# Performance work log

Hardware: AMD Instinct MI355X
Metric: run time of the kernel (lower is better)

Reference implementation:

```python
import jax, jax.numpy as jnp
import numpy as np

B, D1, N, F_IN, F_OUT = 8, 16, 2048, 64, 64


def setup_inputs() -> dict:
    key = jax.random.key(0)
    k1, k2, k3 = jax.random.split(key, 3)
    x = jax.random.normal(k1, (B, D1, N, F_IN), dtype=jnp.float32)
    adj = jax.random.uniform(k2, (B, N, N), dtype=jnp.float32)
    weight = jax.random.normal(k3, (F_IN, F_OUT), dtype=jnp.float32) * (1.0 / np.sqrt(F_IN))
    return {"x": x, "adj": adj, "weight": weight}


def reference(x, adj, weight):
    # x: [B, D1, N, F_in], adj: [B, N, N], weight: [F_in, F_out]
    # Original: per (b, i) loops -> support = x[b,i] @ W; out[b,i] = adj[b] @ support
    # Fused as batched einsums. Note: the module's bias parameter is unused in forward.
    support = jnp.einsum('binf,fg->bing', x, weight)          # feature transform
    out = jnp.einsum('bnm,bimg->bing', adj, support)           # adjacency aggregation
    return out
```

## Files before the change

kernel.cpp:

```cpp
#include <hip/hip_runtime.h>
#include <hip/hip_bf16.h>

typedef __attribute__((ext_vector_type(8))) short bf16x8;
typedef __attribute__((ext_vector_type(4))) float f32x4;

#define NB    8
#define ND1   16
#define NN    2048
#define NF    64
#define GN    1024

__device__ static inline ushort f2bf(float f) {
    unsigned int u = __builtin_bit_cast(unsigned int, f);
    unsigned int r = (u + 0x7FFFu + ((u >> 16) & 1u)) >> 16;
    return (ushort)r;
}

__device__ static inline void gload_lds16(const void* g, void* l) {
    __builtin_amdgcn_global_load_lds(
        (const __attribute__((address_space(1))) void*)g,
        (__attribute__((address_space(3))) void*)l, 16, 0, 0);
}

__global__ __launch_bounds__(256) void prep_kernel(
    const float* __restrict__ x, const float* __restrict__ w,
    const float* __restrict__ adj, ushort* __restrict__ sT,
    ushort* __restrict__ adjb)
{
    __shared__ __align__(16) char smem[16384 + 16640];
    int t = threadIdx.x;

    if (blockIdx.x < 2048) {
        int idx = blockIdx.x * 256 + t;
        const int stride = 2048 * 256;
        const float4* a4 = (const float4*)adj;
        uint4* o4 = (uint4*)adjb;
        const int n8 = NB * NN * NN / 8;
        for (int i = idx; i < n8; i += stride) {
            float4 v0 = a4[2 * i];
            float4 v1 = a4[2 * i + 1];
            union { uint4 q; ushort u[8]; } p;
            p.u[0] = f2bf(v0.x); p.u[1] = f2bf(v0.y);
            p.u[2] = f2bf(v0.z); p.u[3] = f2bf(v0.w);
            p.u[4] = f2bf(v1.x); p.u[5] = f2bf(v1.y);
            p.u[6] = f2bf(v1.z); p.u[7] = f2bf(v1.w);
            o4[i] = p.q;
        }
        return;
    }

    float*  Ws = (float*)smem;
    float*  xs = (float*)(smem + 16384);
    ushort* tr = (ushort*)(smem + 16384);

    int bid = blockIdx.x - 2048;
    int b  = bid >> 9;
    int r  = bid & 511;
    int i  = r >> 5;
    int mb = r & 31;

    const float4* w4 = (const float4*)w;
    const float4* x4 = (const float4*)(x + (((size_t)(b * ND1 + i)) * NN + mb * 64) * NF);
#pragma unroll
    for (int j = 0; j < 4; ++j) {
        float4 wv = w4[j * 256 + t];
        int fl = j * 1024 + t * 4;
        Ws[fl + 0] = wv.x; Ws[fl + 1] = wv.y; Ws[fl + 2] = wv.z; Ws[fl + 3] = wv.w;
        float4 xv = x4[j * 256 + t];
        int ml = fl >> 6, f = fl & 63;
        float* xr = &xs[ml * 65 + f];
        xr[0] = xv.x; xr[1] = xv.y; xr[2] = xv.z; xr[3] = xv.w;
    }
    __syncthreads();

    int ml = t & 63;
    int g0 = (t >> 6) * 16;
    f32x4 acc4[4] = {0.f, 0.f, 0.f, 0.f};
    for (int f = 0; f < 64; ++f) {
        float xv = xs[ml * 65 + f];
        const f32x4* wp = (const f32x4*)&Ws[f * 64 + g0];
#pragma unroll
        for (int q = 0; q < 4; ++q) acc4[q] += xv * wp[q];
    }
    __syncthreads();
#pragma unroll
    for (int j = 0; j < 16; ++j)
        tr[(g0 + j) * 72 + ml] = f2bf(acc4[j >> 2][j & 3]);
    __syncthreads();

    int g = t >> 2, part = t & 3;
    const uint4* src = (const uint4*)&tr[g * 72 + part * 16];
    uint4* dst = (uint4*)(sT + ((size_t)(b * GN + i * 64 + g)) * NN + mb * 64 + part * 16);
    dst[0] = src[0];
    dst[1] = src[1];
}

__global__ __launch_bounds__(512, 2) void gemm8_kernel(
    const ushort* __restrict__ adjb,
    const ushort* __restrict__ sT,
    float* __restrict__ out)
{
    __shared__ __align__(16) ushort lds[65536];

    const int t    = threadIdx.x;
    const int lane = t & 63;
    const int w    = t >> 6;
    const int wm   = w >> 2;
    const int wn   = w & 3;

    int bid  = blockIdx.x;
    int tile = (bid & 7) * 32 + (bid >> 3);
    int b    = tile >> 5;
    int r    = tile & 31;
    int n0   = (r >> 2) * 256;
    int c0   = (r & 3) * 256;

    const ushort* Ab = adjb + (size_t)b * NN * NN + (size_t)n0 * NN;
    const ushort* Bb = sT   + (size_t)b * GN * NN + (size_t)c0 * NN;

    const int rS  = lane & 15;
    const int cgS = lane >> 4;
    const int fq  = ((lane >> 4) * 16 + (lane & 15)) * 8;

    f32x4 acc[8][4];
#pragma unroll
    for (int a = 0; a < 8; ++a)
#pragma unroll
        for (int c = 0; c < 4; ++c) acc[a][c] = (f32x4){0.f, 0.f, 0.f, 0.f};

    auto stg = [&](const ushort* __restrict__ srcb, int tt, int ks, int regionUS) {
#pragma unroll
        for (int j = 0; j < 2; ++j) {
            gload_lds16(srcb + (size_t)((2 * w + j) * 16 + rS) * NN + tt * 64 + ks * 32 + cgS * 8,
                        &lds[regionUS + (2 * w + j) * 512 + lane * 8]);
        }
    };

#define FRAG_A(Ac_, ksoff, ah)                                                  \
    _Pragma("unroll")                                                           \
    for (int a_ = 0; a_ < 4; ++a_)                                              \
        af[a_] = *(const bf16x8*)&lds[(Ac_) + (ksoff) + (wm * 8 + (ah) * 4 + a_) * 512 + fq];
#define FRAG_B(Bc_, ksoff)                                                      \
    _Pragma("unroll")                                                           \
    for (int c_ = 0; c_ < 4; ++c_)                                              \
        bfv[c_] = *(const bf16x8*)&lds[(Bc_) + (ksoff) + (wn * 4 + c_) * 512 + fq];
#define MFMA16(aoff)                                                            \
    __builtin_amdgcn_s_setprio(1);                                              \
    _Pragma("unroll")                                                           \
    for (int a_ = 0; a_ < 4; ++a_)                                              \
        _Pragma("unroll")                                                       \
        for (int c_ = 0; c_ < 4; ++c_)                                          \
            acc[(aoff) + a_][c_] = __builtin_amdgcn_mfma_f32_16x16x32_bf16(     \
                af[a_], bfv[c_], acc[(aoff) + a_][c_], 0, 0, 0);                \
    __builtin_amdgcn_s_setprio(0);
#define BAR() __builtin_amdgcn_s_barrier()
#define LGKM0() asm volatile("s_waitcnt lgkmcnt(0)" ::: "memory")

#define TILE(tt, S12, S34, W2A, W1A)                                            \
    {                                                                           \
        const int buf_ = (tt) & 1;                                              \
        const int Ac = buf_ * 32768, Bc = Ac + 16384;                           \
        const int An = (buf_ ^ 1) * 32768, Bn = An + 16384;                     \
        bf16x8 af[4], bfv[4];                                                   \
                                                 \
        FRAG_A(Ac, 0, 0); FRAG_B(Bc, 0);                                        \
        if (S12) stg(Ab, (tt) + 1, 1, An + 8192);                               \
        BAR(); LGKM0(); MFMA16(0); BAR();                                       \
                                               \
        FRAG_A(Ac, 0, 1);                                                       \
        if (S12) stg(Bb, (tt) + 1, 1, Bn + 8192);                               \
        BAR(); LGKM0(); MFMA16(4);                                              \
        asm volatile(W2A ::: "memory"); BAR();                                  \
                                                 \
        FRAG_A(Ac, 8192, 0); FRAG_B(Bc, 8192);                                  \
        if (S34) stg(Ab, (tt) + 2, 0, Ac);                                      \
        BAR(); LGKM0(); MFMA16(0); BAR();                                       \
                                                          \
        FRAG_A(Ac, 8192, 1);                                                    \
        if (S34) stg(Bb, (tt) + 2, 0, Bc);                                      \
        BAR(); LGKM0(); MFMA16(4);                                              \
        asm volatile(W1A ::: "memory"); BAR();                                  \
    }

    stg(Ab, 0, 0, 0);
    stg(Bb, 0, 0, 16384);
    stg(Ab, 0, 1, 8192);
    stg(Bb, 0, 1, 24576);
    stg(Ab, 1, 0, 32768);
    stg(Bb, 1, 0, 49152);
    asm volatile("s_waitcnt vmcnt(8)" ::: "memory");
    BAR();

    for (int tt = 0; tt < 30; ++tt)
        TILE(tt, 1, 1, "s_waitcnt vmcnt(8)", "s_waitcnt vmcnt(8)");
    TILE(30, 1, 0, "s_waitcnt vmcnt(8)", "s_waitcnt vmcnt(4)");
    TILE(31, 0, 0, "s_waitcnt vmcnt(0)", "");

#pragma unroll
    for (int a = 0; a < 8; ++a) {
        int row0 = n0 + wm * 128 + a * 16 + (lane >> 4) * 4;
#pragma unroll
        for (int c = 0; c < 4; ++c) {
            int col = c0 + wn * 64 + c * 16 + (lane & 15);
            int ii = col >> 6, g = col & 63;
            float* op = out + (((size_t)(b * ND1 + ii)) * NN + row0) * NF + g;
#pragma unroll
            for (int e = 0; e < 4; ++e)
                op[e * NF] = acc[a][c][e];
        }
    }
}

__global__ __launch_bounds__(256) void support_kernel(
    const float* __restrict__ x, const float* __restrict__ w,
    ushort* __restrict__ sT)
{
    __shared__ __align__(16) float Ws[64 * 64];
    __shared__ __align__(16) float xs[64 * 65];
    __shared__ __align__(16) ushort tr[64 * 72];

    int t = threadIdx.x;
    int bid = blockIdx.x;
    int b  = bid >> 9;
    int r  = bid & 511;
    int i  = r >> 5;
    int mb = r & 31;

    const float4* w4 = (const float4*)w;
    const float4* x4 = (const float4*)(x + (((size_t)(b * ND1 + i)) * NN + mb * 64) * NF);
#pragma unroll
    for (int j = 0; j < 4; ++j) {
        float4 wv = w4[j * 256 + t];
        int fl = j * 1024 + t * 4;
        Ws[fl + 0] = wv.x; Ws[fl + 1] = wv.y; Ws[fl + 2] = wv.z; Ws[fl + 3] = wv.w;
        float4 xv = x4[j * 256 + t];
        int ml = fl >> 6, f = fl & 63;
        float* xr = &xs[ml * 65 + f];
        xr[0] = xv.x; xr[1] = xv.y; xr[2] = xv.z; xr[3] = xv.w;
    }
    __syncthreads();

    int ml = t & 63;
    int g0 = (t >> 6) * 16;
    f32x4 acc4[4] = {0.f, 0.f, 0.f, 0.f};
    for (int f = 0; f < 64; ++f) {
        float xv = xs[ml * 65 + f];
        const f32x4* wp = (const f32x4*)&Ws[f * 64 + g0];
#pragma unroll
        for (int q = 0; q < 4; ++q) acc4[q] += xv * wp[q];
    }
#pragma unroll
    for (int j = 0; j < 16; ++j)
        tr[(g0 + j) * 72 + ml] = f2bf(acc4[j >> 2][j & 3]);
    __syncthreads();

    int g = t >> 2, part = t & 3;
    const uint4* src = (const uint4*)&tr[g * 72 + part * 16];
    uint4* dst = (uint4*)(sT + ((size_t)(b * GN + i * 64 + g)) * NN + mb * 64 + part * 16);
    dst[0] = src[0];
    dst[1] = src[1];
}

__global__ __launch_bounds__(256) void gcn_gemm_fb_kernel(
    const float* __restrict__ adjf, const ushort* __restrict__ sT,
    float* __restrict__ out)
{
    __shared__ __align__(16) ushort lA[128 * 64];
    __shared__ __align__(16) ushort lB[128 * 64];

    int t = threadIdx.x;
    int bid0 = blockIdx.x;
    int bid = (bid0 & 7) * 128 + (bid0 >> 3);
    int b  = bid >> 7;
    int rr = bid & 127;
    int n0 = (rr >> 3) * 128;
    int c0 = (rr & 7) * 128;

    const float*  Af = adjf + (size_t)b * NN * NN;
    const ushort* Bb = sT + (size_t)b * GN * NN;

    int lane = t & 63, wv = t >> 6;
    int wr = (wv >> 1) * 64, wc = (wv & 1) * 64;

    f32x4 acc[4][4];
#pragma unroll
    for (int a = 0; a < 4; ++a)
#pragma unroll
        for (int c = 0; c < 4; ++c) acc[a][c] = (f32x4){0.f, 0.f, 0.f, 0.f};

    int sRow = t >> 3;
    int sCol = (t & 7) * 8;

    for (int k0 = 0; k0 < NN; k0 += 64) {
#pragma unroll
        for (int i = 0; i < 4; ++i) {
            const float* src = Af + (size_t)(n0 + i * 32 + sRow) * NN + k0 + sCol;
            float4 v0 = *(const float4*)src;
            float4 v1 = *(const float4*)(src + 4);
            union { bf16x8 v; ushort u[8]; } p;
            p.u[0] = f2bf(v0.x); p.u[1] = f2bf(v0.y);
            p.u[2] = f2bf(v0.z); p.u[3] = f2bf(v0.w);
            p.u[4] = f2bf(v1.x); p.u[5] = f2bf(v1.y);
            p.u[6] = f2bf(v1.z); p.u[7] = f2bf(v1.w);
            *(bf16x8*)&lA[(i * 32 + sRow) * 64 + sCol] = p.v;
        }
#pragma unroll
        for (int i = 0; i < 4; ++i)
            gload_lds16(Bb + (size_t)(c0 + i * 32 + sRow) * NN + k0 + sCol,
                        &lB[(i * 32 + sRow) * 64 + sCol]);
        __syncthreads();
#pragma unroll
        for (int kk = 0; kk < 2; ++kk) {
            bf16x8 af[4], bfr[4];
#pragma unroll
            for (int a = 0; a < 4; ++a)
                af[a] = *(const bf16x8*)&lA[(wr + a * 16 + (lane & 15)) * 64 + kk * 32 + (lane >> 4) * 8];
#pragma unroll
            for (int c = 0; c < 4; ++c)
                bfr[c] = *(const bf16x8*)&lB[(wc + c * 16 + (lane & 15)) * 64 + kk * 32 + (lane >> 4) * 8];
#pragma unroll
            for (int a = 0; a < 4; ++a)
#pragma unroll
                for (int c = 0; c < 4; ++c)
                    acc[a][c] = __builtin_amdgcn_mfma_f32_16x16x32_bf16(af[a], bfr[c], acc[a][c], 0, 0, 0);
        }
        __syncthreads();
    }
#pragma unroll
    for (int a = 0; a < 4; ++a) {
        int row0 = n0 + wr + a * 16 + (lane >> 4) * 4;
#pragma unroll
        for (int c = 0; c < 4; ++c) {
            int col = c0 + wc + c * 16 + (lane & 15);
            int ii = col >> 6, g = col & 63;
            float* op = out + (((size_t)(b * ND1 + ii)) * NN + row0) * NF + g;
#pragma unroll
            for (int e = 0; e < 4; ++e)
                op[e * NF] = acc[a][c][e];
        }
    }
}

extern "C" void kernel_launch(void* const* d_in, const int* in_sizes, int n_in,
                              void* d_out, int out_size, void* d_ws, size_t ws_size,
                              hipStream_t stream) {
    const float* x   = (const float*)d_in[0];
    const float* adj = (const float*)d_in[1];
    const float* w   = (const float*)d_in[2];
    float* out = (float*)d_out;

    ushort* sT   = (ushort*)d_ws;
    ushort* adjb = (ushort*)((char*)d_ws + 33554432);
    bool preconv = ws_size >= (size_t)100663296;

    if (preconv) {
        prep_kernel<<<dim3(6144), dim3(256), 0, stream>>>(x, w, adj, sT, adjb);
        gemm8_kernel<<<dim3(256), dim3(512), 0, stream>>>(adjb, sT, out);
    } else {
        support_kernel<<<dim3(NB * ND1 * (NN / 64)), dim3(256), 0, stream>>>(x, w, sT);
        gcn_gemm_fb_kernel<<<dim3(NB * 16 * 8), dim3(256), 0, stream>>>(adj, sT, out);
    }
}
```

Before: 354.5 us.

## Compute support transform with bf16 MFMA in registers, reorder prep blocks

The support computation (x @ W) in prep_kernel moves from an LDS-staged fp32 scalar FMA loop to bf16 MFMA 16x16x32 instructions with W fragments held in registers. Each block now covers 512 rows with four waves of 128 rows each, instead of 64 rows per block, which cuts the block count and removes LDS use and barriers. The support blocks are now launched first, ahead of the adjacency conversion blocks. The trade-off is that x is rounded to bf16 before the multiply, and the transposed output is written as scattered 2-byte stores rather than coalesced 16-byte ones.

```diff
diff --git a/kernel.cpp b/kernel.cpp
--- a/kernel.cpp
+++ b/kernel.cpp
@@ -27,11 +27,10 @@
     const float* __restrict__ adj, ushort* __restrict__ sT,
     ushort* __restrict__ adjb)
 {
-    __shared__ __align__(16) char smem[16384 + 16640];
     int t = threadIdx.x;
 
-    if (blockIdx.x < 2048) {
-        int idx = blockIdx.x * 256 + t;
+    if (blockIdx.x >= 512) {
+        int idx = (blockIdx.x - 512) * 256 + t;
         const int stride = 2048 * 256;
         const float4* a4 = (const float4*)adj;
         uint4* o4 = (uint4*)adjb;
@@ -49,50 +48,69 @@
         return;
     }
 
-    float*  Ws = (float*)smem;
-    float*  xs = (float*)(smem + 16384);
-    ushort* tr = (ushort*)(smem + 16384);
-
-    int bid = blockIdx.x - 2048;
-    int b  = bid >> 9;
-    int r  = bid & 511;
-    int i  = r >> 5;
-    int mb = r & 31;
-
-    const float4* w4 = (const float4*)w;
-    const float4* x4 = (const float4*)(x + (((size_t)(b * ND1 + i)) * NN + mb * 64) * NF);
-#pragma unroll
-    for (int j = 0; j < 4; ++j) {
-        float4 wv = w4[j * 256 + t];
-        int fl = j * 1024 + t * 4;
-        Ws[fl + 0] = wv.x; Ws[fl + 1] = wv.y; Ws[fl + 2] = wv.z; Ws[fl + 3] = wv.w;
-        float4 xv = x4[j * 256 + t];
-        int ml = fl >> 6, f = fl & 63;
-        float* xr = &xs[ml * 65 + f];
-        xr[0] = xv.x; xr[1] = xv.y; xr[2] = xv.z; xr[3] = xv.w;
-    }
-    __syncthreads();
-
-    int ml = t & 63;
-    int g0 = (t >> 6) * 16;
-    f32x4 acc4[4] = {0.f, 0.f, 0.f, 0.f};
-    for (int f = 0; f < 64; ++f) {
-        float xv = xs[ml * 65 + f];
-        const f32x4* wp = (const f32x4*)&Ws[f * 64 + g0];
-#pragma unroll
-        for (int q = 0; q < 4; ++q) acc4[q] += xv * wp[q];
-    }
-    __syncthreads();
-#pragma unroll
-    for (int j = 0; j < 16; ++j)
-        tr[(g0 + j) * 72 + ml] = f2bf(acc4[j >> 2][j & 3]);
-    __syncthreads();
-
-    int g = t >> 2, part = t & 3;
-    const uint4* src = (const uint4*)&tr[g * 72 + part * 16];
-    uint4* dst = (uint4*)(sT + ((size_t)(b * GN + i * 64 + g)) * NN + mb * 64 + part * 16);
-    dst[0] = src[0];
-    dst[1] = src[1];
+    int q    = blockIdx.x;
+    int b    = q >> 6;
+    int i    = (q >> 2) & 15;
+    int quar = q & 3;
+    int lane = t & 63;
+    int wid  = t >> 6;
+    int mwave = quar * 512 + wid * 128;
+
+    const float* xp = x + ((size_t)(b * ND1 + i)) * NN * NF;
+    ushort* outp = sT + ((size_t)(b * GN) + i * 64) * NN;
+
+    const int r16 = lane & 15;
+    const int kq  = lane >> 4;
+
+    bf16x8 afr[4][2];
+#pragma unroll
+    for (int gt = 0; gt < 4; ++gt)
+#pragma unroll
+        for (int kk = 0; kk < 2; ++kk) {
+            union { bf16x8 v; ushort u[8]; } pk;
+#pragma unroll
+            for (int j = 0; j < 8; ++j) {
+                int f = kk * 32 + kq * 8 + j;
+                pk.u[j] = f2bf(w[f * 64 + gt * 16 + r16]);
+            }
+            afr[gt][kk] = pk.v;
+        }
+
+    for (int mt = 0; mt < 8; ++mt) {
+        int m0 = mwave + mt * 16;
+        const float* xr = xp + (size_t)(m0 + r16) * NF;
+
+        bf16x8 bfr[2];
+#pragma unroll
+        for (int kk = 0; kk < 2; ++kk) {
+            float4 v0 = *(const float4*)(xr + kk * 32 + kq * 8);
+            float4 v1 = *(const float4*)(xr + kk * 32 + kq * 8 + 4);
+            union { bf16x8 v; ushort u[8]; } pk;
+            pk.u[0] = f2bf(v0.x); pk.u[1] = f2bf(v0.y);
+            pk.u[2] = f2bf(v0.z); pk.u[3] = f2bf(v0.w);
+            pk.u[4] = f2bf(v1.x); pk.u[5] = f2bf(v1.y);
+            pk.u[6] = f2bf(v1.z); pk.u[7] = f2bf(v1.w);
+            bfr[kk] = pk.v;
+        }
+
+        f32x4 acc[4];
+#pragma unroll
+        for (int gt = 0; gt < 4; ++gt) acc[gt] = (f32x4){0.f, 0.f, 0.f, 0.f};
+#pragma unroll
+        for (int gt = 0; gt < 4; ++gt)
+#pragma unroll
+            for (int kk = 0; kk < 2; ++kk)
+                acc[gt] = __builtin_amdgcn_mfma_f32_16x16x32_bf16(
+                    afr[gt][kk], bfr[kk], acc[gt], 0, 0, 0);
+
+#pragma unroll
+        for (int gt = 0; gt < 4; ++gt)
+#pragma unroll
+            for (int e = 0; e < 4; ++e) {
+                int g = gt * 16 + kq * 4 + e;
+                outp[(size_t)g * NN + m0 + r16] = f2bf(acc[gt][e]);
+            }
+    }
 }
 
 __global__ __launch_bounds__(512, 2) void gemm8_kernel(
@@ -162,20 +180,16 @@
         const int Ac = buf_ * 32768, Bc = Ac + 16384;                           \
         const int An = (buf_ ^ 1) * 32768, Bn = An + 16384;                     \
         bf16x8 af[4], bfv[4];                                                   \
-                                                 \
         FRAG_A(Ac, 0, 0); FRAG_B(Bc, 0);                                        \
         if (S12) stg(Ab, (tt) + 1, 1, An + 8192);                               \
         BAR(); LGKM0(); MFMA16(0); BAR();                                       \
-                                               \
         FRAG_A(Ac, 0, 1);                                                       \
         if (S12) stg(Bb, (tt) + 1, 1, Bn + 8192);                               \
         BAR(); LGKM0(); MFMA16(4);                                              \
         asm volatile(W2A ::: "memory"); BAR();                                  \
-                                                 \
         FRAG_A(Ac, 8192, 0); FRAG_B(Bc, 8192);                                  \
         if (S34) stg(Ab, (tt) + 2, 0, Ac);                                      \
         BAR(); LGKM0(); MFMA16(0); BAR();                                       \
-                                                          \
         FRAG_A(Ac, 8192, 1);                                                    \
         if (S34) stg(Bb, (tt) + 2, 0, Bc);                                      \
         BAR(); LGKM0(); MFMA16(4);                                              \
@@ -354,7 +368,7 @@
     bool preconv = ws_size >= (size_t)100663296;
 
     if (preconv) {
-        prep_kernel<<<dim3(6144), dim3(256), 0, stream>>>(x, w, adj, sT, adjb);
+        prep_kernel<<<dim3(2560), dim3(256), 0, stream>>>(x, w, adj, sT, adjb);
         gemm8_kernel<<<dim3(256), dim3(512), 0, stream>>>(adjb, sT, out);
     } else {
         support_kernel<<<dim3(NB * ND1 * (NN / 64)), dim3(256), 0, stream>>>(x, w, sT);
```

Result: slower. 366.1 us (+3.3%).
